# Kernel optimization log

Measured on AMD Instinct MI355X. Metric: run time of the kernel, lower is better.

The kernel has to match this reference:

```python
import jax, jax.numpy as jnp
import numpy as np

B, N, D, M, DEPTH, VOCAB = 8, 128, 128, 16, 4, 100
EIN = 2 * D + 1          # edge MLP input dim: feats_i | feats_j | rel_dist
LN_EPS = 1e-5


def setup_inputs() -> dict:
    key = jax.random.key(0)
    ks = jax.random.split(key, 20)
    s = 0.02  # small init like egnn-pytorch's init_eps
    f32 = jnp.float32
    return {
        "z": jax.random.randint(ks[0], (B, N), 0, VOCAB),
        "pos": jax.random.normal(ks[1], (B, N, 3), f32),
        "mask": jnp.ones((B, N), bool),
        "emb": jax.random.normal(ks[2], (VOCAB, D), f32) * s,
        # edge MLP: Linear(EIN, 2*EIN) -> SiLU -> Linear(2*EIN, M) -> SiLU
        "e_w1": jax.random.normal(ks[3], (DEPTH, EIN, 2 * EIN), f32) * s,
        "e_b1": jnp.zeros((DEPTH, 2 * EIN), f32),
        "e_w2": jax.random.normal(ks[4], (DEPTH, 2 * EIN, M), f32) * s,
        "e_b2": jnp.zeros((DEPTH, M), f32),
        # coors MLP: Linear(M, 4M) -> SiLU -> Linear(4M, 1)
        "c_w1": jax.random.normal(ks[5], (DEPTH, M, 4 * M), f32) * s,
        "c_b1": jnp.zeros((DEPTH, 4 * M), f32),
        "c_w2": jax.random.normal(ks[6], (DEPTH, 4 * M, 1), f32) * s,
        "c_b2": jnp.zeros((DEPTH, 1), f32),
        # node LayerNorm (norm_feats=True in EGNN_Network)
        "ln_g": jnp.ones((DEPTH, D), f32),
        "ln_b": jnp.zeros((DEPTH, D), f32),
        # node MLP: Linear(D+M, 2D) -> SiLU -> Linear(2D, D), residual
        "n_w1": jax.random.normal(ks[7], (DEPTH, D + M, 2 * D), f32) * s,
        "n_b1": jnp.zeros((DEPTH, 2 * D), f32),
        "n_w2": jax.random.normal(ks[8], (DEPTH, 2 * D, D), f32) * s,
        "n_b2": jnp.zeros((DEPTH, D), f32),
    }


def _egnn_forward(z, pos, mask, emb, e_w1, e_b1, e_w2, e_b2,
                  c_w1, c_b1, c_w2, c_b2, ln_g, ln_b,
                  n_w1, n_b1, n_w2, n_b2):
    feats = emb[z]                       # [B,N,D]
    coors = pos                          # [B,N,3]
    mf = mask.astype(feats.dtype)        # [B,N]
    pair = mf[:, :, None] * mf[:, None, :]   # [B,N,N] pairwise mask
    for l in range(DEPTH):
        rel = coors[:, :, None, :] - coors[:, None, :, :]       # [B,N,N,3]
        dist = jnp.sum(rel * rel, axis=-1, keepdims=True)       # [B,N,N,1]
        fi = jnp.broadcast_to(feats[:, :, None, :], (B, N, N, D))
        fj = jnp.broadcast_to(feats[:, None, :, :], (B, N, N, D))
        e = jnp.concatenate([fi, fj, dist], axis=-1)             # [B,N,N,EIN]
        h = jax.nn.silu(e @ e_w1[l] + e_b1[l])                   # [B,N,N,2*EIN]
        m_ij = jax.nn.silu(h @ e_w2[l] + e_b2[l])                # [B,N,N,M]
        # coordinate update
        cw = (jax.nn.silu(m_ij @ c_w1[l] + c_b1[l]) @ c_w2[l] + c_b2[l])[..., 0]
        cw = cw * pair                                           # mask invalid pairs
        coors = coors + jnp.einsum('bij,bijc->bic', cw, rel)
        # node update: masked sum-pool of messages over j
        m_i = jnp.sum(m_ij * pair[..., None], axis=2)            # [B,N,M]
        mu = jnp.mean(feats, axis=-1, keepdims=True)
        var = jnp.var(feats, axis=-1, keepdims=True)
        fn = (feats - mu) * jax.lax.rsqrt(var + LN_EPS) * ln_g[l] + ln_b[l]
        ni = jnp.concatenate([fn, m_i], axis=-1)                 # [B,N,D+M]
        feats = feats + (jax.nn.silu(ni @ n_w1[l] + n_b1[l]) @ n_w2[l] + n_b2[l])
    # masked mean pool
    w = mf[..., None]
    return jnp.sum(feats * w, axis=1) / jnp.maximum(jnp.sum(w, axis=1), 1.0)


def reference(z, pos, mask, emb, e_w1, e_b1, e_w2, e_b2,
              c_w1, c_b1, c_w2, c_b2, ln_g, ln_b,
              n_w1, n_b1, n_w2, n_b2):
    return _egnn_forward(z, pos, mask, emb, e_w1, e_b1, e_w2, e_b2,
                         c_w1, c_b1, c_w2, c_b2, ln_g, ln_b,
                         n_w1, n_b1, n_w2, n_b2)
```

## Files before the change

kernel.cpp:

```cpp
#include <hip/hip_runtime.h>

#define BATCH 8
#define NN    128
#define DD    128
#define MM    16
#define DEPTH 4
#define EIN   257
#define H1    514
#define KPAD  544
#define NCH   17
#define NODES (BATCH*NN)
#define BQ_B  69632
#define NL2E  (-1.442695040888963f)
#define NLN2  (-0.6931471805599453f)

typedef __attribute__((ext_vector_type(8))) short short8;
typedef __attribute__((ext_vector_type(4))) float floatx4;

__device__ __forceinline__ float b2f(unsigned short u) {
    return __uint_as_float(((unsigned int)u) << 16);
}
__device__ __forceinline__ unsigned short f2b(float f) {
    unsigned int x = __float_as_uint(f);
    unsigned int r = (x + 0x7fffu + ((x >> 16) & 1u)) >> 16;
    return (unsigned short)r;
}
__device__ __forceinline__ float siluf(float x) {
    float t = __builtin_amdgcn_exp2f(x * NL2E);
    return x * __builtin_amdgcn_rcpf(1.0f + t);
}
__device__ __forceinline__ float loadf(const void* p, size_t idx, int isbf) {
    return isbf ? b2f(((const unsigned short*)p)[idx]) : ((const float*)p)[idx];
}
__device__ __forceinline__ unsigned int pk2(float x, float y) {
    unsigned int xb = __float_as_uint(x) + 0x8000u;
    unsigned int yb = __float_as_uint(y) + 0x8000u;
    return __builtin_amdgcn_perm(yb, xb, 0x07060302);
}
__device__ __forceinline__ unsigned int h2pk_y(float y0, float y1) {
    float t0 = __builtin_amdgcn_exp2f(y0);
    float t1 = __builtin_amdgcn_exp2f(y1);
    float h0 = y0 * __builtin_amdgcn_rcpf(1.0f + t0);
    float h1 = y1 * __builtin_amdgcn_rcpf(1.0f + t1);
    return pk2(h0, h1);
}

#define OFF_FEATS   0
#define OFF_COORSA  131072
#define OFF_COORSB  134144
#define OFF_AB      137216
#define OFF_BQ      694272
#define OFF_CPK     1267712
#define OFF_WLB     1272576
#define OFF_W2F     1274816
#define OFF_FLAG    1292224
#define OFF_FB16    1292228
#define OFF_W1F     1357764
#define OFF_CF      1636352
#define OFF_NW1F    1640448
#define OFF_NW2F    1722368
#define OFF_NI      1787904

__global__ __launch_bounds__(256) void k_init(
    const int* __restrict__ z, const void* __restrict__ pos,
    const void* __restrict__ emb,
    const void* __restrict__ e_w1, const void* __restrict__ e_w2,
    const void* __restrict__ e_b2,
    const void* __restrict__ c_w1, const void* __restrict__ c_b1,
    const void* __restrict__ c_w2, const void* __restrict__ c_b2,
    const void* __restrict__ n_w1, const void* __restrict__ n_w2,
    float* __restrict__ feats, unsigned short* __restrict__ fb16,
    float* __restrict__ coorsA,
    float* __restrict__ wlb, int4* __restrict__ w2frag,
    int4* __restrict__ w1frag,
    float* __restrict__ cpack, int4* __restrict__ cfrag,
    int4* __restrict__ nw1f, int4* __restrict__ nw2f,
    int* __restrict__ flag) {
    __shared__ int sfl;
    int tid = threadIdx.x, bx = blockIdx.x;
    if (tid < 64) {
        float f = fabsf(__uint_as_float(((const unsigned int*)pos)[tid]));
        bool ok = (f == 0.f) || (f > 1e-8f && f < 1e8f);
        unsigned long long v = __ballot(ok);
        if (tid == 0) sfl = (__builtin_popcountll(v) >= 32) ? 0 : 1;
    }
    __syncthreads();
    int isbf = sfl;
    if (bx == 0 && tid == 0) *flag = isbf;
    if (bx < 512) {
        int node = 2 * bx + (tid >> 7), t = tid & 127;
        int zi = z[node];
        float v = loadf(emb, (size_t)zi * DD + t, isbf);
        feats[node * DD + t] = v;
        fb16[node * DD + t] = f2b(v);
        if (t < 3) coorsA[node * 3 + t] = loadf(pos, node * 3 + t, isbf);
    } else if (bx < 580) {
        int p = bx - 512;
        int layer = p / NCH, kc = p % NCH;
        if (tid < 64) {
            int quad = tid >> 4, c = tid & 15;
            size_t w2base = (size_t)layer * H1 * MM;
            unsigned int u[4];
            #pragma unroll
            for (int pp = 0; pp < 4; ++pp) {
                int k0 = kc * 32 + quad * 8 + 2 * pp, k1 = k0 + 1;
                float f0 = (k0 < H1) ? loadf(e_w2, w2base + (size_t)k0 * MM + c, isbf) : 0.f;
                float f1 = (k1 < H1) ? loadf(e_w2, w2base + (size_t)k1 * MM + c, isbf) : 0.f;
                u[pp] = pk2(f0, f1);
            }
            w2frag[(layer * NCH + kc) * 64 + tid] =
                make_int4((int)u[0], (int)u[1], (int)u[2], (int)u[3]);
            if (kc == 0) {
                size_t wlbase = ((size_t)layer * EIN + 256) * H1;
                for (int t = tid; t < KPAD; t += 64)
                    wlb[layer * 560 + t] =
                        (t < H1) ? NL2E * loadf(e_w1, wlbase + t, isbf) : 0.f;
                if (tid < 16)
                    wlb[layer * 560 + 544 + tid] = loadf(e_b2, layer * MM + tid, isbf);
            }
        }
    } else if (bx < 584) {
        int l = bx - 580;
        for (int idx = tid; idx < 1024; idx += 256) {
            int c = idx >> 6, hh = idx & 63;
            cpack[l * 1216 + hh * 16 + c] = loadf(c_w1, l * 1024 + c * 64 + hh, isbf);
        }
        if (tid < 64)        cpack[l * 1216 + 1024 + tid] = loadf(c_b1, l * 64 + tid, isbf);
        else if (tid < 128)  cpack[l * 1216 + 1088 + tid - 64] = loadf(c_w2, l * 64 + tid - 64, isbf);
        else if (tid == 128) cpack[l * 1216 + 1152] = loadf(c_b2, l, isbf);
        {
            int nt = tid >> 6, lane = tid & 63;
            int col = nt * 16 + (lane & 15);
            unsigned int u[4];
            #pragma unroll
            for (int pp = 0; pp < 4; ++pp) {
                int k0 = (lane >> 4) * 8 + 2 * pp;
                float f0 = (k0 < 16)     ? loadf(c_w1, (size_t)l * 1024 + (size_t)k0 * 64 + col, isbf) : 0.f;
                float f1 = (k0 + 1 < 16) ? loadf(c_w1, (size_t)l * 1024 + (size_t)(k0 + 1) * 64 + col, isbf) : 0.f;
                u[pp] = pk2(f0, f1);
            }
            cfrag[((size_t)l * 4 + nt) * 64 + lane] =
                make_int4((int)u[0], (int)u[1], (int)u[2], (int)u[3]);
        }
    } else if (bx < 856) {
        int p = bx - 584;
        int l = p / 68, nt = p % 68;
        int kcd = tid >> 6, lane = tid & 63;
        int quad = lane >> 4, c16 = lane & 15;
        int n_local = nt * 16 + c16;
        int half = n_local >= KPAD;
        int k_out = n_local - (half ? KPAD : 0);
        size_t wbase = (size_t)l * EIN * H1 + (size_t)(half ? 128 : 0) * H1 + k_out;
        unsigned int u[4];
        #pragma unroll
        for (int pp = 0; pp < 4; ++pp) {
            int d0 = kcd * 32 + quad * 8 + 2 * pp;
            float f0 = (k_out < H1) ? loadf(e_w1, wbase + (size_t)d0 * H1, isbf) : 0.f;
            float f1 = (k_out < H1) ? loadf(e_w1, wbase + (size_t)(d0 + 1) * H1, isbf) : 0.f;
            u[pp] = pk2(f0, f1);
        }
        w1frag[((size_t)(l * 68 + nt) * 4 + kcd) * 64 + lane] =
            make_int4((int)u[0], (int)u[1], (int)u[2], (int)u[3]);
    } else if (bx < 876) {
        int p = bx - 856, l = p / 5, kc = p % 5;
        int lane = tid & 63;
        for (int nt = tid >> 6; nt < 16; nt += 4) {
            int col = nt * 16 + (lane & 15);
            unsigned int u[4];
            #pragma unroll
            for (int pp = 0; pp < 4; ++pp) {
                int k0 = kc * 32 + (lane >> 4) * 8 + 2 * pp;
                float f0 = (k0 < 144)
                    ? loadf(n_w1, (size_t)l * 144 * 256 + (size_t)k0 * 256 + col, isbf) : 0.f;
                float f1 = (k0 + 1 < 144)
                    ? loadf(n_w1, (size_t)l * 144 * 256 + (size_t)(k0 + 1) * 256 + col, isbf) : 0.f;
                u[pp] = pk2(f0, f1);
            }
            nw1f[((size_t)(l * 5 + kc) * 16 + nt) * 64 + lane] =
                make_int4((int)u[0], (int)u[1], (int)u[2], (int)u[3]);
        }
    } else {
        int p = bx - 876, l = p / 8, kc = p % 8;
        int lane = tid & 63;
        for (int nt = tid >> 6; nt < 8; nt += 4) {
            int col = nt * 16 + (lane & 15);
            unsigned int u[4];
            #pragma unroll
            for (int pp = 0; pp < 4; ++pp) {
                int k0 = kc * 32 + (lane >> 4) * 8 + 2 * pp;
                float f0 = loadf(n_w2, (size_t)l * 256 * 128 + (size_t)k0 * 128 + col, isbf);
                float f1 = loadf(n_w2, (size_t)l * 256 * 128 + (size_t)(k0 + 1) * 128 + col, isbf);
                u[pp] = pk2(f0, f1);
            }
            nw2f[((size_t)(l * 8 + kc) * 8 + nt) * 64 + lane] =
                make_int4((int)u[0], (int)u[1], (int)u[2], (int)u[3]);
        }
    }
}

__global__ __launch_bounds__(256) void k1_ab(
    const unsigned short* __restrict__ fb16, const int4* __restrict__ w1f,
    const void* __restrict__ b1raw, unsigned int b1off,
    float* __restrict__ Ab, float* __restrict__ Bq,
    const int* __restrict__ flagp) {
    int bx = blockIdx.x;
    int mt = bx & 63, ng = bx >> 6;
    int tid = threadIdx.x, w = tid >> 6, lane = tid & 63;
    int quad = lane >> 4, c16 = lane & 15;
    int isbf = *flagp;
    int ntile = ng * 4 + w;
    int n_local = ntile * 16 + c16;
    int half = n_local >= KPAD;
    int k_out = n_local - (half ? KPAD : 0);

    const unsigned short* ap = fb16 + (size_t)(mt * 16 + c16) * DD + quad * 8;
    const int4* bp = w1f + (size_t)ntile * 4 * 64 + lane;
    floatx4 acc = {0.f, 0.f, 0.f, 0.f};
    #pragma unroll
    for (int kcd = 0; kcd < 4; ++kcd) {
        short8 af = *(const short8*)(ap + kcd * 32);
        union { int4 i4; short8 s; } bf;
        bf.i4 = bp[kcd * 64];
        acc = __builtin_amdgcn_mfma_f32_16x16x32_bf16(af, bf.s, acc, 0, 0, 0);
    }
    if (!half) {
        float bias = (k_out < H1) ? loadf(b1raw, b1off + k_out, isbf) : 0.f;
        #pragma unroll
        for (int r = 0; r < 4; ++r)
            Ab[(size_t)(mt * 16 + quad * 4 + r) * KPAD + k_out] =
                NL2E * (acc[r] + bias);
    } else {
        int kc = k_out >> 5, kk = k_out & 31;
        int qd = kk >> 3, hsel = (kk >> 2) & 1, tt = k_out & 3;
        #pragma unroll
        for (int r = 0; r < 4; ++r) {
            int node = mt * 16 + quad * 4 + r;
            int bb = node >> 7, j = node & 127;
            int jt = j >> 4, lj = qd * 16 + (j & 15);
            Bq[(size_t)bb * BQ_B + kc * 4096 + jt * 512 + hsel * 256
               + lj * 4 + tt] = NL2E * acc[r];
        }
    }
}

__global__ __launch_bounds__(512, 6) void k2_node(
    const float* __restrict__ Ab, const float* __restrict__ Bq,
    const float* __restrict__ coorsIn, float* __restrict__ coorsOut,
    const float* __restrict__ feats, unsigned short* __restrict__ niB,
    const float* __restrict__ wlbL,
    const short8* __restrict__ w2fragL,
    const float* __restrict__ cpk,
    const int4* __restrict__ cfL,
    const void* __restrict__ gln, const void* __restrict__ bln,
    unsigned int layer, const int* __restrict__ flagp) {
    __shared__ float Ms[128 * 17];
    __shared__ float px[128], py[128], pz[128];
    __shared__ float msum[16][16];
    __shared__ float cwf[128];
    __shared__ float red[2][3];
    __shared__ float fr[128];
    __shared__ float ni[144];
    int tid = threadIdx.x;
    int b = blockIdx.x & 7, ii = blockIdx.x >> 3;
    int node0 = b * NN + ii;
    int w = tid >> 6, lane = tid & 63;
    int quad = lane >> 4, c16 = lane & 15;
    int kg = w >> 2, wj = w & 3;
    int isbf = *flagp;

    if (tid < 128) {
        int g = (b * NN + tid) * 3;
        px[tid] = coorsIn[g]; py[tid] = coorsIn[g + 1]; pz[tid] = coorsIn[g + 2];
    } else if (tid < 256) {
        int t = tid - 128;
        fr[t] = feats[(size_t)node0 * DD + t];
    }
    __syncthreads();

    int j0 = wj * 16 + c16, j1 = j0 + 64;
    float pix = px[ii], piy = py[ii], piz = pz[ii];
    float dxa = pix - px[j0], dya = piy - py[j0], dza = piz - pz[j0];
    float d2a = dxa*dxa + dya*dya + dza*dza;
    float dxb = pix - px[j1], dyb = piy - py[j1], dzb = piz - pz[j1];
    float d2b = dxb*dxb + dyb*dyb + dzb*dzb;
    float b2v = wlbL[544 + c16];

    const float* arow = Ab + (size_t)node0 * KPAD + quad * 8;
    const float* wlr  = wlbL + quad * 8;
    const float* bqw  = Bq + (size_t)b * BQ_B + wj * 512 + lane * 4;
    const short8* wfp = w2fragL + lane;

    floatx4 acc0 = {0.f,0.f,0.f,0.f}, acc1 = {0.f,0.f,0.f,0.f};

    int kc0 = kg ? 9 : 0, kc1 = kg ? 17 : 9;
    {
        const float* bqp = bqw + (size_t)kc0 * 4096;
        float4 npp0 = *(const float4*)(bqp);
        float4 npp1 = *(const float4*)(bqp + 256);
        float4 nqq0 = *(const float4*)(bqp + 2048);
        float4 nqq1 = *(const float4*)(bqp + 2304);
        short8 nbf  = wfp[kc0 * 64];
        for (int kc = kc0; kc < kc1; ++kc) {
            float4 pp0 = npp0, pp1 = npp1, qq0 = nqq0, qq1 = nqq1;
            short8 bf = nbf;
            const float* bqn = bqw + (size_t)(kc + 1) * 4096;
            npp0 = *(const float4*)(bqn);
            npp1 = *(const float4*)(bqn + 256);
            nqq0 = *(const float4*)(bqn + 2048);
            nqq1 = *(const float4*)(bqn + 2304);
            nbf  = wfp[(kc + 1) * 64];
            float4 aA0 = *(const float4*)(arow + kc * 32);
            float4 aA1 = *(const float4*)(arow + kc * 32 + 4);
            float4 l0  = *(const float4*)(wlr + kc * 32);
            float4 l1  = *(const float4*)(wlr + kc * 32 + 4);
            union { unsigned int u[4]; short8 s; } ua, ub;
            ua.u[0] = h2pk_y(fmaf(d2a, l0.x, aA0.x + pp0.x),
                             fmaf(d2a, l0.y, aA0.y + pp0.y));
            ua.u[1] = h2pk_y(fmaf(d2a, l0.z, aA0.z + pp0.z),
                             fmaf(d2a, l0.w, aA0.w + pp0.w));
            ua.u[2] = h2pk_y(fmaf(d2a, l1.x, aA1.x + pp1.x),
                             fmaf(d2a, l1.y, aA1.y + pp1.y));
            ua.u[3] = h2pk_y(fmaf(d2a, l1.z, aA1.z + pp1.z),
                             fmaf(d2a, l1.w, aA1.w + pp1.w));
            ub.u[0] = h2pk_y(fmaf(d2b, l0.x, aA0.x + qq0.x),
                             fmaf(d2b, l0.y, aA0.y + qq0.y));
            ub.u[1] = h2pk_y(fmaf(d2b, l0.z, aA0.z + qq0.z),
                             fmaf(d2b, l0.w, aA0.w + qq0.w));
            ub.u[2] = h2pk_y(fmaf(d2b, l1.x, aA1.x + qq1.x),
                             fmaf(d2b, l1.y, aA1.y + qq1.y));
            ub.u[3] = h2pk_y(fmaf(d2b, l1.z, aA1.z + qq1.z),
                             fmaf(d2b, l1.w, aA1.w + qq1.w));
            acc0 = __builtin_amdgcn_mfma_f32_16x16x32_bf16(ua.s, bf, acc0, 0, 0, 0);
            acc1 = __builtin_amdgcn_mfma_f32_16x16x32_bf16(ub.s, bf, acc1, 0, 0, 0);
        }
    }

    if (kg == 0) {
        #pragma unroll
        for (int r = 0; r < 4; ++r) {
            int jl = (wj * 16 + quad * 4 + r) * 17 + c16;
            Ms[jl]           = acc0[r];
            Ms[jl + 64 * 17] = acc1[r];
        }
    }
    __syncthreads();
    if (kg == 1) {
        #pragma unroll
        for (int r = 0; r < 4; ++r) {
            int jl = (wj * 16 + quad * 4 + r) * 17 + c16;
            Ms[jl]           = siluf(fmaf(Ms[jl]           + acc0[r], NLN2, b2v));
            Ms[jl + 64 * 17] = siluf(fmaf(Ms[jl + 64 * 17] + acc1[r], NLN2, b2v));
        }
    }
    __syncthreads();

    if (tid < 256) {
        int g = tid >> 4, c = tid & 15;
        float s = 0.f;
        #pragma unroll
        for (int t = 0; t < 8; ++t) s += Ms[(g * 8 + t) * 17 + c];
        msum[g][c] = s;
    }
    __syncthreads();

    if (tid < 16) {
        float s = 0.f;
        #pragma unroll
        for (int g = 0; g < 16; ++g) s += msum[g][tid];
        ni[128 + tid] = s;
    }
    if (tid < 64) {
        int l6 = tid;
        unsigned int lnoff = layer * DD;
        float v0 = fr[l6], v1 = fr[l6 + 64];
        float s1 = v0 + v1, s2 = v0 * v0 + v1 * v1;
        #pragma unroll
        for (int off = 32; off >= 1; off >>= 1) {
            s1 += __shfl_xor(s1, off, 64);
            s2 += __shfl_xor(s2, off, 64);
        }
        float mu  = s1 * (1.0f / 128.0f);
        float var = s2 * (1.0f / 128.0f) - mu * mu;
        float rs  = rsqrtf(var + 1e-5f);
        ni[l6]      = (v0 - mu) * rs * loadf(gln, lnoff + l6, isbf)
                    + loadf(bln, lnoff + l6, isbf);
        ni[l6 + 64] = (v1 - mu) * rs * loadf(gln, lnoff + l6 + 64, isbf)
                    + loadf(bln, lnoff + l6 + 64, isbf);
    }

    {
        int l15 = lane & 15, l4 = lane >> 4;
        union { unsigned int u[4]; short8 s; } am;
        if (l4 < 2) {
            const float* msp = &Ms[(w * 16 + l15) * 17 + l4 * 8];
            am.u[0] = pk2(msp[0], msp[1]);
            am.u[1] = pk2(msp[2], msp[3]);
            am.u[2] = pk2(msp[4], msp[5]);
            am.u[3] = pk2(msp[6], msp[7]);
        } else {
            am.u[0] = am.u[1] = am.u[2] = am.u[3] = 0u;
        }
        floatx4 ca0 = {0.f,0.f,0.f,0.f}, ca1 = {0.f,0.f,0.f,0.f},
                ca2 = {0.f,0.f,0.f,0.f}, ca3 = {0.f,0.f,0.f,0.f};
        union { int4 i4; short8 s; } cb;
        cb.i4 = cfL[0 * 64 + lane];
        ca0 = __builtin_amdgcn_mfma_f32_16x16x32_bf16(am.s, cb.s, ca0, 0, 0, 0);
        cb.i4 = cfL[1 * 64 + lane];
        ca1 = __builtin_amdgcn_mfma_f32_16x16x32_bf16(am.s, cb.s, ca1, 0, 0, 0);
        cb.i4 = cfL[2 * 64 + lane];
        ca2 = __builtin_amdgcn_mfma_f32_16x16x32_bf16(am.s, cb.s, ca2, 0, 0, 0);
        cb.i4 = cfL[3 * 64 + lane];
        ca3 = __builtin_amdgcn_mfma_f32_16x16x32_bf16(am.s, cb.s, ca3, 0, 0, 0);
        float cb1v0 = cpk[1024 + l15],      cw2v0 = cpk[1088 + l15];
        float cb1v1 = cpk[1024 + 16 + l15], cw2v1 = cpk[1088 + 16 + l15];
        float cb1v2 = cpk[1024 + 32 + l15], cw2v2 = cpk[1088 + 32 + l15];
        float cb1v3 = cpk[1024 + 48 + l15], cw2v3 = cpk[1088 + 48 + l15];
        float cwp[4];
        #pragma unroll
        for (int r = 0; r < 4; ++r) {
            cwp[r] = siluf(ca0[r] + cb1v0) * cw2v0
                   + siluf(ca1[r] + cb1v1) * cw2v1
                   + siluf(ca2[r] + cb1v2) * cw2v2
                   + siluf(ca3[r] + cb1v3) * cw2v3;
        }
        #pragma unroll
        for (int off = 1; off <= 8; off <<= 1) {
            #pragma unroll
            for (int r = 0; r < 4; ++r) cwp[r] += __shfl_xor(cwp[r], off, 64);
        }
        if (l15 == 0) {
            float cb2v = cpk[1152];
            #pragma unroll
            for (int r = 0; r < 4; ++r)
                cwf[w * 16 + l4 * 4 + r] = cwp[r] + cb2v;
        }
    }
    __syncthreads();

    if (tid < 128) {
        int j = tid;
        float cw = cwf[j];
        float vx = cw * (pix - px[j]), vy = cw * (piy - py[j]),
              vz = cw * (piz - pz[j]);
        #pragma unroll
        for (int off = 32; off >= 1; off >>= 1) {
            vx += __shfl_xor(vx, off, 64);
            vy += __shfl_xor(vy, off, 64);
            vz += __shfl_xor(vz, off, 64);
        }
        if (lane == 0) { red[w][0] = vx; red[w][1] = vy; red[w][2] = vz; }
    } else if (tid < 288) {
        int t = tid - 128;
        niB[(size_t)node0 * 160 + t] = (t < 144) ? f2b(ni[t]) : (unsigned short)0;
    }
    __syncthreads();

    if (tid < 3) {
        coorsOut[node0 * 3 + tid] = coorsIn[node0 * 3 + tid]
            + red[0][tid] + red[1][tid];
    }
}

__global__ __launch_bounds__(256) void k3_node(
    const unsigned short* __restrict__ niB,
    const int4* __restrict__ nw1f, const int4* __restrict__ nw2f,
    const void* __restrict__ b1r, const void* __restrict__ b2r,
    float* __restrict__ feats, unsigned short* __restrict__ fb16,
    unsigned int layer, const int* __restrict__ flagp) {
    __shared__ float hid[16][260];
    int tid = threadIdx.x, m = blockIdx.x;
    int w = tid >> 6, lane = tid & 63;
    int l15 = lane & 15, l4 = lane >> 4;
    int isbf = *flagp;

    floatx4 acc0 = {0.f,0.f,0.f,0.f}, acc1 = {0.f,0.f,0.f,0.f},
            acc2 = {0.f,0.f,0.f,0.f}, acc3 = {0.f,0.f,0.f,0.f};
    const unsigned short* nip = niB + (size_t)(m * 16 + l15) * 160 + l4 * 8;
    const int4* b1p = nw1f + (size_t)layer * 5 * 16 * 64 + lane;
    #pragma unroll
    for (int kc = 0; kc < 5; ++kc) {
        short8 af = *(const short8*)(nip + kc * 32);
        union { int4 i4; short8 s; } bf;
        bf.i4 = b1p[(kc * 16 + w * 4 + 0) * 64];
        acc0 = __builtin_amdgcn_mfma_f32_16x16x32_bf16(af, bf.s, acc0, 0, 0, 0);
        bf.i4 = b1p[(kc * 16 + w * 4 + 1) * 64];
        acc1 = __builtin_amdgcn_mfma_f32_16x16x32_bf16(af, bf.s, acc1, 0, 0, 0);
        bf.i4 = b1p[(kc * 16 + w * 4 + 2) * 64];
        acc2 = __builtin_amdgcn_mfma_f32_16x16x32_bf16(af, bf.s, acc2, 0, 0, 0);
        bf.i4 = b1p[(kc * 16 + w * 4 + 3) * 64];
        acc3 = __builtin_amdgcn_mfma_f32_16x16x32_bf16(af, bf.s, acc3, 0, 0, 0);
    }
    {
        int h0 = (w * 4) * 16 + l15;
        float b1v0 = loadf(b1r, layer * 256 + h0, isbf);
        float b1v1 = loadf(b1r, layer * 256 + h0 + 16, isbf);
        float b1v2 = loadf(b1r, layer * 256 + h0 + 32, isbf);
        float b1v3 = loadf(b1r, layer * 256 + h0 + 48, isbf);
        #pragma unroll
        for (int r = 0; r < 4; ++r) {
            int row = l4 * 4 + r;
            hid[row][h0]      = siluf(acc0[r] + b1v0);
            hid[row][h0 + 16] = siluf(acc1[r] + b1v1);
            hid[row][h0 + 32] = siluf(acc2[r] + b1v2);
            hid[row][h0 + 48] = siluf(acc3[r] + b1v3);
        }
    }
    __syncthreads();

    floatx4 o0 = {0.f,0.f,0.f,0.f}, o1 = {0.f,0.f,0.f,0.f};
    const int4* b2p = nw2f + (size_t)layer * 8 * 8 * 64 + lane;
    #pragma unroll
    for (int kc = 0; kc < 8; ++kc) {
        const float* hp = &hid[l15][kc * 32 + l4 * 8];
        float4 h0 = *(const float4*)(hp);
        float4 h1 = *(const float4*)(hp + 4);
        union { unsigned int u[4]; short8 s; } af;
        af.u[0] = pk2(h0.x, h0.y); af.u[1] = pk2(h0.z, h0.w);
        af.u[2] = pk2(h1.x, h1.y); af.u[3] = pk2(h1.z, h1.w);
        union { int4 i4; short8 s; } bf;
        bf.i4 = b2p[(kc * 8 + w * 2 + 0) * 64];
        o0 = __builtin_amdgcn_mfma_f32_16x16x32_bf16(af.s, bf.s, o0, 0, 0, 0);
        bf.i4 = b2p[(kc * 8 + w * 2 + 1) * 64];
        o1 = __builtin_amdgcn_mfma_f32_16x16x32_bf16(af.s, bf.s, o1, 0, 0, 0);
    }
    {
        int c0 = (w * 2) * 16 + l15;
        float b2v0 = loadf(b2r, layer * 128 + c0, isbf);
        float b2v1 = loadf(b2r, layer * 128 + c0 + 16, isbf);
        #pragma unroll
        for (int r = 0; r < 4; ++r) {
            int node = m * 16 + l4 * 4 + r;
            float v0 = feats[(size_t)node * DD + c0] + o0[r] + b2v0;
            float v1 = feats[(size_t)node * DD + c0 + 16] + o1[r] + b2v1;
            feats[(size_t)node * DD + c0]      = v0;
            feats[(size_t)node * DD + c0 + 16] = v1;
            fb16[(size_t)node * DD + c0]       = f2b(v0);
            fb16[(size_t)node * DD + c0 + 16]  = f2b(v1);
        }
    }
}

__global__ __launch_bounds__(128) void k4_pool(
    const float* __restrict__ feats, void* __restrict__ out,
    const int* __restrict__ flagp) {
    int b = blockIdx.x, d = threadIdx.x;
    float s = 0.f;
    for (int n = 0; n < NN; ++n) s += feats[((size_t)(b * NN + n)) * DD + d];
    float v = s * (1.0f / 128.0f);
    if (*flagp) ((unsigned short*)out)[b * DD + d] = f2b(v);
    else        ((float*)out)[b * DD + d] = v;
}

extern "C" void kernel_launch(void* const* d_in, const int* in_sizes, int n_in,
                              void* d_out, int out_size, void* d_ws, size_t ws_size,
                              hipStream_t stream) {
    const int* z = (const int*)d_in[0];
    const void* pos  = d_in[1];
    const void* emb  = d_in[3];
    const void* e_w1 = d_in[4];
    const void* e_b1 = d_in[5];
    const void* e_w2 = d_in[6];
    const void* e_b2 = d_in[7];
    const void* c_w1 = d_in[8];
    const void* c_b1 = d_in[9];
    const void* c_w2 = d_in[10];
    const void* c_b2 = d_in[11];
    const void* ln_g = d_in[12];
    const void* ln_b = d_in[13];
    const void* n_w1 = d_in[14];
    const void* n_b1 = d_in[15];
    const void* n_w2 = d_in[16];
    const void* n_b2 = d_in[17];

    float* ws     = (float*)d_ws;
    float* feats  = ws + OFF_FEATS;
    float* coorsA = ws + OFF_COORSA;
    float* coorsB = ws + OFF_COORSB;
    float* Ab     = ws + OFF_AB;
    float* Bq     = ws + OFF_BQ;
    float* cpk    = ws + OFF_CPK;
    float* wlb    = ws + OFF_WLB;
    int4*  w2f    = (int4*)(ws + OFF_W2F);
    int*   flag   = (int*)(ws + OFF_FLAG);
    unsigned short* fb16 = (unsigned short*)(ws + OFF_FB16);
    int4*  w1f    = (int4*)(ws + OFF_W1F);
    int4*  cf     = (int4*)(ws + OFF_CF);
    int4*  nw1f   = (int4*)(ws + OFF_NW1F);
    int4*  nw2f   = (int4*)(ws + OFF_NW2F);
    unsigned short* niB = (unsigned short*)(ws + OFF_NI);

    k_init<<<908, 256, 0, stream>>>(
        z, pos, emb, e_w1, e_w2, e_b2, c_w1, c_b1, c_w2, c_b2, n_w1, n_w2,
        feats, fb16, coorsA, wlb, w2f, w1f, cpk, cf, nw1f, nw2f, flag);

    float* cin = coorsA; float* cout = coorsB;
    for (int l = 0; l < DEPTH; ++l) {
        k1_ab<<<1088, 256, 0, stream>>>(
            fb16, w1f + (size_t)l * 68 * 4 * 64, e_b1,
            (unsigned int)(l * H1), Ab, Bq, flag);
        k2_node<<<NODES, 512, 0, stream>>>(
            Ab, Bq, cin, cout, feats, niB,
            wlb + l * 560, (const short8*)(w2f + (size_t)l * NCH * 64),
            cpk + (size_t)l * 1216, cf + (size_t)l * 4 * 64,
            ln_g, ln_b, (unsigned int)l, flag);
        k3_node<<<NODES / 16, 256, 0, stream>>>(
            niB, nw1f, nw2f, n_b1, n_b2, feats, fb16,
            (unsigned int)l, flag);
        float* t = cin; cin = cout; cout = t;
    }
    k4_pool<<<BATCH, 128, 0, stream>>>(feats, d_out, flag);
}
```

Before: 254.2 us.

## Fuse node MLP into next layer's edge projection and pair two nodes per block

Fuses the node-update MLP (k3) with the next layer's Ab/Bq edge-projection (k1) into one kernel. Each of the 17 column-group blocks recomputes the 16-node MLP redundantly, which removes a launch and the fb16 round trip. Feats are now ping-ponged between two buffers so the redundant blocks can read old feats safely. The pair kernel now handles two i-nodes per block, reusing the Bq and weight-fragment loads across both, and replaces the msum reduction with shuffles plus fewer syncs. The cost is heavy redundant MLP compute in the fused kernel and more registers in k2, whose occupancy hint drops from 6 to 4.

```diff
diff --git a/kernel.cpp b/kernel.cpp
--- a/kernel.cpp
+++ b/kernel.cpp
@@ -60,6 +60,7 @@
 #define OFF_NW1F    1640448
 #define OFF_NW2F    1722368
 #define OFF_NI      1787904
+#define OFF_FEATS2  1869824
 
 __global__ __launch_bounds__(256) void k_init(
     const int* __restrict__ z, const void* __restrict__ pos,
@@ -243,26 +244,146 @@
     }
 }
 
-__global__ __launch_bounds__(512, 6) void k2_node(
+__global__ __launch_bounds__(256) void k13(
+    const unsigned short* __restrict__ niB,
+    const int4* __restrict__ nw1f, const int4* __restrict__ nw2f,
+    const void* __restrict__ nb1, const void* __restrict__ nb2,
+    const float* __restrict__ featsIn, float* __restrict__ featsOut,
+    const int4* __restrict__ w1f, const void* __restrict__ b1raw,
+    unsigned int b1off, float* __restrict__ Ab, float* __restrict__ Bq,
+    unsigned int lm1, const int* __restrict__ flagp) {
+    __shared__ float hid[16][260];
+    __shared__ unsigned short fbt[16][136];
+    int tid = threadIdx.x, bx = blockIdx.x;
+    int mt = bx & 63, ng = bx >> 6;
+    int w = tid >> 6, lane = tid & 63;
+    int l15 = lane & 15, l4 = lane >> 4;
+    int isbf = *flagp;
+
+    floatx4 acc0 = {0.f,0.f,0.f,0.f}, acc1 = {0.f,0.f,0.f,0.f},
+            acc2 = {0.f,0.f,0.f,0.f}, acc3 = {0.f,0.f,0.f,0.f};
+    const unsigned short* nip = niB + (size_t)(mt * 16 + l15) * 160 + l4 * 8;
+    const int4* b1p = nw1f + (size_t)lm1 * 5 * 16 * 64 + lane;
+    #pragma unroll
+    for (int kc = 0; kc < 5; ++kc) {
+        short8 af = *(const short8*)(nip + kc * 32);
+        union { int4 i4; short8 s; } bf;
+        bf.i4 = b1p[(kc * 16 + w * 4 + 0) * 64];
+        acc0 = __builtin_amdgcn_mfma_f32_16x16x32_bf16(af, bf.s, acc0, 0, 0, 0);
+        bf.i4 = b1p[(kc * 16 + w * 4 + 1) * 64];
+        acc1 = __builtin_amdgcn_mfma_f32_16x16x32_bf16(af, bf.s, acc1, 0, 0, 0);
+        bf.i4 = b1p[(kc * 16 + w * 4 + 2) * 64];
+        acc2 = __builtin_amdgcn_mfma_f32_16x16x32_bf16(af, bf.s, acc2, 0, 0, 0);
+        bf.i4 = b1p[(kc * 16 + w * 4 + 3) * 64];
+        acc3 = __builtin_amdgcn_mfma_f32_16x16x32_bf16(af, bf.s, acc3, 0, 0, 0);
+    }
+    {
+        int h0 = (w * 4) * 16 + l15;
+        float b1v0 = loadf(nb1, lm1 * 256 + h0, isbf);
+        float b1v1 = loadf(nb1, lm1 * 256 + h0 + 16, isbf);
+        float b1v2 = loadf(nb1, lm1 * 256 + h0 + 32, isbf);
+        float b1v3 = loadf(nb1, lm1 * 256 + h0 + 48, isbf);
+        #pragma unroll
+        for (int r = 0; r < 4; ++r) {
+            int row = l4 * 4 + r;
+            hid[row][h0]      = siluf(acc0[r] + b1v0);
+            hid[row][h0 + 16] = siluf(acc1[r] + b1v1);
+            hid[row][h0 + 32] = siluf(acc2[r] + b1v2);
+            hid[row][h0 + 48] = siluf(acc3[r] + b1v3);
+        }
+    }
+    __syncthreads();
+
+    floatx4 o0 = {0.f,0.f,0.f,0.f}, o1 = {0.f,0.f,0.f,0.f};
+    const int4* b2p = nw2f + (size_t)lm1 * 8 * 8 * 64 + lane;
+    #pragma unroll
+    for (int kc = 0; kc < 8; ++kc) {
+        const float* hp = &hid[l15][kc * 32 + l4 * 8];
+        float4 h0 = *(const float4*)(hp);
+        float4 h1 = *(const float4*)(hp + 4);
+        union { unsigned int u[4]; short8 s; } af;
+        af.u[0] = pk2(h0.x, h0.y); af.u[1] = pk2(h0.z, h0.w);
+        af.u[2] = pk2(h1.x, h1.y); af.u[3] = pk2(h1.z, h1.w);
+        union { int4 i4; short8 s; } bf;
+        bf.i4 = b2p[(kc * 8 + w * 2 + 0) * 64];
+        o0 = __builtin_amdgcn_mfma_f32_16x16x32_bf16(af.s, bf.s, o0, 0, 0, 0);
+        bf.i4 = b2p[(kc * 8 + w * 2 + 1) * 64];
+        o1 = __builtin_amdgcn_mfma_f32_16x16x32_bf16(af.s, bf.s, o1, 0, 0, 0);
+    }
+    {
+        int c0 = (w * 2) * 16 + l15;
+        float b2v0 = loadf(nb2, lm1 * 128 + c0, isbf);
+        float b2v1 = loadf(nb2, lm1 * 128 + c0 + 16, isbf);
+        #pragma unroll
+        for (int r = 0; r < 4; ++r) {
+            int row = l4 * 4 + r;
+            int node = mt * 16 + row;
+            float v0 = featsIn[(size_t)node * DD + c0] + o0[r] + b2v0;
+            float v1 = featsIn[(size_t)node * DD + c0 + 16] + o1[r] + b2v1;
+            fbt[row][c0]      = f2b(v0);
+            fbt[row][c0 + 16] = f2b(v1);
+            if (ng == 0) {
+                featsOut[(size_t)node * DD + c0]      = v0;
+                featsOut[(size_t)node * DD + c0 + 16] = v1;
+            }
+        }
+    }
+    __syncthreads();
+
+    int quad = l4, c16 = l15;
+    int ntile = ng * 4 + w;
+    int n_local = ntile * 16 + c16;
+    int half = n_local >= KPAD;
+    int k_out = n_local - (half ? KPAD : 0);
+    const int4* bp = w1f + (size_t)ntile * 4 * 64 + lane;
+    floatx4 acc = {0.f, 0.f, 0.f, 0.f};
+    #pragma unroll
+    for (int kcd = 0; kcd < 4; ++kcd) {
+        short8 af = *(const short8*)(&fbt[c16][quad * 8 + kcd * 32]);
+        union { int4 i4; short8 s; } bf;
+        bf.i4 = bp[kcd * 64];
+        acc = __builtin_amdgcn_mfma_f32_16x16x32_bf16(af, bf.s, acc, 0, 0, 0);
+    }
+    if (!half) {
+        float bias = (k_out < H1) ? loadf(b1raw, b1off + k_out, isbf) : 0.f;
+        #pragma unroll
+        for (int r = 0; r < 4; ++r)
+            Ab[(size_t)(mt * 16 + quad * 4 + r) * KPAD + k_out] =
+                NL2E * (acc[r] + bias);
+    } else {
+        int kc = k_out >> 5, kk = k_out & 31;
+        int qd = kk >> 3, hsel = (kk >> 2) & 1, tt = k_out & 3;
+        #pragma unroll
+        for (int r = 0; r < 4; ++r) {
+            int node = mt * 16 + quad * 4 + r;
+            int bb = node >> 7, j = node & 127;
+            int jt = j >> 4, lj = qd * 16 + (j & 15);
+            Bq[(size_t)bb * BQ_B + kc * 4096 + jt * 512 + hsel * 256
+               + lj * 4 + tt] = NL2E * acc[r];
+        }
+    }
+}
+
+__global__ __launch_bounds__(512, 4) void k2_pair(
     const float* __restrict__ Ab, const float* __restrict__ Bq,
     const float* __restrict__ coorsIn, float* __restrict__ coorsOut,
-    const float* __restrict__ feats, unsigned short* __restrict__ niB,
+    const float* __restrict__ featsIn, unsigned short* __restrict__ niB,
     const float* __restrict__ wlbL,
     const short8* __restrict__ w2fragL,
     const float* __restrict__ cpk,
     const int4* __restrict__ cfL,
     const void* __restrict__ gln, const void* __restrict__ bln,
     unsigned int layer, const int* __restrict__ flagp) {
-    __shared__ float Ms[128 * 17];
+    __shared__ float Ms[2][128 * 17];
     __shared__ float px[128], py[128], pz[128];
-    __shared__ float msum[16][16];
-    __shared__ float cwf[128];
-    __shared__ float red[2][3];
-    __shared__ float fr[128];
-    __shared__ float ni[144];
+    __shared__ float msum[2][4][16];
+    __shared__ float cwf[2][128];
+    __shared__ float fr[2][128];
+    __shared__ float ni[2][144];
     int tid = threadIdx.x;
-    int b = blockIdx.x & 7, ii = blockIdx.x >> 3;
-    int node0 = b * NN + ii;
+    int b = blockIdx.x & 7, ip = blockIdx.x >> 3;
+    int i0 = ip * 2;
+    int node0 = b * NN + i0;
     int w = tid >> 6, lane = tid & 63;
     int quad = lane >> 4, c16 = lane & 15;
     int kg = w >> 2, wj = w & 3;
@@ -271,26 +392,34 @@
     if (tid < 128) {
         int g = (b * NN + tid) * 3;
         px[tid] = coorsIn[g]; py[tid] = coorsIn[g + 1]; pz[tid] = coorsIn[g + 2];
-    } else if (tid < 256) {
-        int t = tid - 128;
-        fr[t] = feats[(size_t)node0 * DD + t];
+    } else if (tid < 384) {
+        int n = (tid - 128) >> 7, t = tid & 127;
+        fr[n][t] = featsIn[(size_t)(node0 + n) * DD + t];
     }
     __syncthreads();
 
     int j0 = wj * 16 + c16, j1 = j0 + 64;
-    float pix = px[ii], piy = py[ii], piz = pz[ii];
-    float dxa = pix - px[j0], dya = piy - py[j0], dza = piz - pz[j0];
-    float d2a = dxa*dxa + dya*dya + dza*dza;
-    float dxb = pix - px[j1], dyb = piy - py[j1], dzb = piz - pz[j1];
-    float d2b = dxb*dxb + dyb*dyb + dzb*dzb;
+    float pix0 = px[i0],     piy0 = py[i0],     piz0 = pz[i0];
+    float pix1 = px[i0 + 1], piy1 = py[i0 + 1], piz1 = pz[i0 + 1];
+    float dx, dy, dz;
+    dx = pix0 - px[j0]; dy = piy0 - py[j0]; dz = piz0 - pz[j0];
+    float d2a0 = dx*dx + dy*dy + dz*dz;
+    dx = pix0 - px[j1]; dy = piy0 - py[j1]; dz = piz0 - pz[j1];
+    float d2b0 = dx*dx + dy*dy + dz*dz;
+    dx = pix1 - px[j0]; dy = piy1 - py[j0]; dz = piz1 - pz[j0];
+    float d2a1 = dx*dx + dy*dy + dz*dz;
+    dx = pix1 - px[j1]; dy = piy1 - py[j1]; dz = piz1 - pz[j1];
+    float d2b1 = dx*dx + dy*dy + dz*dz;
     float b2v = wlbL[544 + c16];
 
-    const float* arow = Ab + (size_t)node0 * KPAD + quad * 8;
-    const float* wlr  = wlbL + quad * 8;
-    const float* bqw  = Bq + (size_t)b * BQ_B + wj * 512 + lane * 4;
-    const short8* wfp = w2fragL + lane;
-
-    floatx4 acc0 = {0.f,0.f,0.f,0.f}, acc1 = {0.f,0.f,0.f,0.f};
+    const float* arow0 = Ab + (size_t)node0 * KPAD + quad * 8;
+    const float* arow1 = arow0 + KPAD;
+    const float* wlr   = wlbL + quad * 8;
+    const float* bqw   = Bq + (size_t)b * BQ_B + wj * 512 + lane * 4;
+    const short8* wfp  = w2fragL + lane;
+
+    floatx4 acc00 = {0.f,0.f,0.f,0.f}, acc01 = {0.f,0.f,0.f,0.f};
+    floatx4 acc10 = {0.f,0.f,0.f,0.f}, acc11 = {0.f,0.f,0.f,0.f};
 
     int kc0 = kg ? 9 : 0, kc1 = kg ? 17 : 9;
     {
@@ -309,29 +438,49 @@
             nqq0 = *(const float4*)(bqn + 2048);
             nqq1 = *(const float4*)(bqn + 2304);
             nbf  = wfp[(kc + 1) * 64];
-            float4 aA0 = *(const float4*)(arow + kc * 32);
-            float4 aA1 = *(const float4*)(arow + kc * 32 + 4);
+            float4 aA0 = *(const float4*)(arow0 + kc * 32);
+            float4 aA1 = *(const float4*)(arow0 + kc * 32 + 4);
+            float4 aB0 = *(const float4*)(arow1 + kc * 32);
+            float4 aB1 = *(const float4*)(arow1 + kc * 32 + 4);
             float4 l0  = *(const float4*)(wlr + kc * 32);
             float4 l1  = *(const float4*)(wlr + kc * 32 + 4);
-            union { unsigned int u[4]; short8 s; } ua, ub;
-            ua.u[0] = h2pk_y(fmaf(d2a, l0.x, aA0.x + pp0.x),
-                             fmaf(d2a, l0.y, aA0.y + pp0.y));
-            ua.u[1] = h2pk_y(fmaf(d2a, l0.z, aA0.z + pp0.z),
-                             fmaf(d2a, l0.w, aA0.w + pp0.w));
-            ua.u[2] = h2pk_y(fmaf(d2a, l1.x, aA1.x + pp1.x),
-                             fmaf(d2a, l1.y, aA1.y + pp1.y));
-            ua.u[3] = h2pk_y(fmaf(d2a, l1.z, aA1.z + pp1.z),
-                             fmaf(d2a, l1.w, aA1.w + pp1.w));
-            ub.u[0] = h2pk_y(fmaf(d2b, l0.x, aA0.x + qq0.x),
-                             fmaf(d2b, l0.y, aA0.y + qq0.y));
-            ub.u[1] = h2pk_y(fmaf(d2b, l0.z, aA0.z + qq0.z),
-                             fmaf(d2b, l0.w, aA0.w + qq0.w));
-            ub.u[2] = h2pk_y(fmaf(d2b, l1.x, aA1.x + qq1.x),
-                             fmaf(d2b, l1.y, aA1.y + qq1.y));
-            ub.u[3] = h2pk_y(fmaf(d2b, l1.z, aA1.z + qq1.z),
-                             fmaf(d2b, l1.w, aA1.w + qq1.w));
-            acc0 = __builtin_amdgcn_mfma_f32_16x16x32_bf16(ua.s, bf, acc0, 0, 0, 0);
-            acc1 = __builtin_amdgcn_mfma_f32_16x16x32_bf16(ub.s, bf, acc1, 0, 0, 0);
+            union { unsigned int u[4]; short8 s; } ua, ub, uc, ud;
+            ua.u[0] = h2pk_y(fmaf(d2a0, l0.x, aA0.x + pp0.x),
+                             fmaf(d2a0, l0.y, aA0.y + pp0.y));
+            ua.u[1] = h2pk_y(fmaf(d2a0, l0.z, aA0.z + pp0.z),
+                             fmaf(d2a0, l0.w, aA0.w + pp0.w));
+            ua.u[2] = h2pk_y(fmaf(d2a0, l1.x, aA1.x + pp1.x),
+                             fmaf(d2a0, l1.y, aA1.y + pp1.y));
+            ua.u[3] = h2pk_y(fmaf(d2a0, l1.z, aA1.z + pp1.z),
+                             fmaf(d2a0, l1.w, aA1.w + pp1.w));
+            ub.u[0] = h2pk_y(fmaf(d2b0, l0.x, aA0.x + qq0.x),
+                             fmaf(d2b0, l0.y, aA0.y + qq0.y));
+            ub.u[1] = h2pk_y(fmaf(d2b0, l0.z, aA0.z + qq0.z),
+                             fmaf(d2b0, l0.w, aA0.w + qq0.w));
+            ub.u[2] = h2pk_y(fmaf(d2b0, l1.x, aA1.x + qq1.x),
+                             fmaf(d2b0, l1.y, aA1.y + qq1.y));
+            ub.u[3] = h2pk_y(fmaf(d2b0, l1.z, aA1.z + qq1.z),
+                             fmaf(d2b0, l1.w, aA1.w + qq1.w));
+            uc.u[0] = h2pk_y(fmaf(d2a1, l0.x, aB0.x + pp0.x),
+                             fmaf(d2a1, l0.y, aB0.y + pp0.y));
+            uc.u[1] = h2pk_y(fmaf(d2a1, l0.z, aB0.z + pp0.z),
+                             fmaf(d2a1, l0.w, aB0.w + pp0.w));
+            uc.u[2] = h2pk_y(fmaf(d2a1, l1.x, aB1.x + pp1.x),
+                             fmaf(d2a1, l1.y, aB1.y + pp1.y));
+            uc.u[3] = h2pk_y(fmaf(d2a1, l1.z, aB1.z + pp1.z),
+                             fmaf(d2a1, l1.w, aB1.w + pp1.w));
+            ud.u[0] = h2pk_y(fmaf(d2b1, l0.x, aB0.x + qq0.x),
+                             fmaf(d2b1, l0.y, aB0.y + qq0.y));
+            ud.u[1] = h2pk_y(fmaf(d2b1, l0.z, aB0.z + qq0.z),
+                             fmaf(d2b1, l0.w, aB0.w + qq0.w));
+            ud.u[2] = h2pk_y(fmaf(d2b1, l1.x, aB1.x + qq1.x),
+                             fmaf(d2b1, l1.y, aB1.y + qq1.y));
+            ud.u[3] = h2pk_y(fmaf(d2b1, l1.z, aB1.z + qq1.z),
+                             fmaf(d2b1, l1.w, aB1.w + qq1.w));
+            acc00 = __builtin_amdgcn_mfma_f32_16x16x32_bf16(ua.s, bf, acc00, 0, 0, 0);
+            acc01 = __builtin_amdgcn_mfma_f32_16x16x32_bf16(ub.s, bf, acc01, 0, 0, 0);
+            acc10 = __builtin_amdgcn_mfma_f32_16x16x32_bf16(uc.s, bf, acc10, 0, 0, 0);
+            acc11 = __builtin_amdgcn_mfma_f32_16x16x32_bf16(ud.s, bf, acc11, 0, 0, 0);
         }
     }
 
@@ -339,40 +488,35 @@
         #pragma unroll
         for (int r = 0; r < 4; ++r) {
             int jl = (wj * 16 + quad * 4 + r) * 17 + c16;
-            Ms[jl]           = acc0[r];
-            Ms[jl + 64 * 17] = acc1[r];
+            Ms[0][jl]        = acc00[r];
+            Ms[0][jl + 1088] = acc01[r];
+            Ms[1][jl]        = acc10[r];
+            Ms[1][jl + 1088] = acc11[r];
         }
     }
     __syncthreads();
+
     if (kg == 1) {
+        float s0 = 0.f, s1 = 0.f;
         #pragma unroll
         for (int r = 0; r < 4; ++r) {
             int jl = (wj * 16 + quad * 4 + r) * 17 + c16;
-            Ms[jl]           = siluf(fmaf(Ms[jl]           + acc0[r], NLN2, b2v));
-            Ms[jl + 64 * 17] = siluf(fmaf(Ms[jl + 64 * 17] + acc1[r], NLN2, b2v));
-        }
-    }
-    __syncthreads();
-
-    if (tid < 256) {
-        int g = tid >> 4, c = tid & 15;
-        float s = 0.f;
-        #pragma unroll
-        for (int t = 0; t < 8; ++t) s += Ms[(g * 8 + t) * 17 + c];
-        msum[g][c] = s;
-    }
-    __syncthreads();
-
-    if (tid < 16) {
-        float s = 0.f;
-        #pragma unroll
-        for (int g = 0; g < 16; ++g) s += msum[g][tid];
-        ni[128 + tid] = s;
-    }
-    if (tid < 64) {
-        int l6 = tid;
+            float m00 = siluf(fmaf(Ms[0][jl]        + acc00[r], NLN2, b2v));
+            float m01 = siluf(fmaf(Ms[0][jl + 1088] + acc01[r], NLN2, b2v));
+            float m10 = siluf(fmaf(Ms[1][jl]        + acc10[r], NLN2, b2v));
+            float m11 = siluf(fmaf(Ms[1][jl + 1088] + acc11[r], NLN2, b2v));
+            Ms[0][jl] = m00; Ms[0][jl + 1088] = m01;
+            Ms[1][jl] = m10; Ms[1][jl + 1088] = m11;
+            s0 += m00 + m01;
+            s1 += m10 + m11;
+        }
+        s0 += __shfl_xor(s0, 16, 64); s0 += __shfl_xor(s0, 32, 64);
+        s1 += __shfl_xor(s1, 16, 64); s1 += __shfl_xor(s1, 32, 64);
+        if (quad == 0) { msum[0][wj][c16] = s0; msum[1][wj][c16] = s1; }
+    } else if (w < 2) {
+        int n = w, l6 = lane;
         unsigned int lnoff = layer * DD;
-        float v0 = fr[l6], v1 = fr[l6 + 64];
+        float v0 = fr[n][l6], v1 = fr[n][l6 + 64];
         float s1 = v0 + v1, s2 = v0 * v0 + v1 * v1;
         #pragma unroll
         for (int off = 32; off >= 1; off >>= 1) {
@@ -382,91 +526,108 @@
         float mu  = s1 * (1.0f / 128.0f);
         float var = s2 * (1.0f / 128.0f) - mu * mu;
         float rs  = rsqrtf(var + 1e-5f);
-        ni[l6]      = (v0 - mu) * rs * loadf(gln, lnoff + l6, isbf)
-                    + loadf(bln, lnoff + l6, isbf);
-        ni[l6 + 64] = (v1 - mu) * rs * loadf(gln, lnoff + l6 + 64, isbf)
-                    + loadf(bln, lnoff + l6 + 64, isbf);
-    }
+        ni[n][l6]      = (v0 - mu) * rs * loadf(gln, lnoff + l6, isbf)
+                       + loadf(bln, lnoff + l6, isbf);
+        ni[n][l6 + 64] = (v1 - mu) * rs * loadf(gln, lnoff + l6 + 64, isbf)
+                       + loadf(bln, lnoff + l6 + 64, isbf);
+    }
+    __syncthreads();
 
     {
         int l15 = lane & 15, l4 = lane >> 4;
-        union { unsigned int u[4]; short8 s; } am;
-        if (l4 < 2) {
-            const float* msp = &Ms[(w * 16 + l15) * 17 + l4 * 8];
-            am.u[0] = pk2(msp[0], msp[1]);
-            am.u[1] = pk2(msp[2], msp[3]);
-            am.u[2] = pk2(msp[4], msp[5]);
-            am.u[3] = pk2(msp[6], msp[7]);
-        } else {
-            am.u[0] = am.u[1] = am.u[2] = am.u[3] = 0u;
-        }
-        floatx4 ca0 = {0.f,0.f,0.f,0.f}, ca1 = {0.f,0.f,0.f,0.f},
-                ca2 = {0.f,0.f,0.f,0.f}, ca3 = {0.f,0.f,0.f,0.f};
-        union { int4 i4; short8 s; } cb;
-        cb.i4 = cfL[0 * 64 + lane];
-        ca0 = __builtin_amdgcn_mfma_f32_16x16x32_bf16(am.s, cb.s, ca0, 0, 0, 0);
-        cb.i4 = cfL[1 * 64 + lane];
-        ca1 = __builtin_amdgcn_mfma_f32_16x16x32_bf16(am.s, cb.s, ca1, 0, 0, 0);
-        cb.i4 = cfL[2 * 64 + lane];
-        ca2 = __builtin_amdgcn_mfma_f32_16x16x32_bf16(am.s, cb.s, ca2, 0, 0, 0);
-        cb.i4 = cfL[3 * 64 + lane];
-        ca3 = __builtin_amdgcn_mfma_f32_16x16x32_bf16(am.s, cb.s, ca3, 0, 0, 0);
+        int nw = w >> 2;
         float cb1v0 = cpk[1024 + l15],      cw2v0 = cpk[1088 + l15];
         float cb1v1 = cpk[1024 + 16 + l15], cw2v1 = cpk[1088 + 16 + l15];
         float cb1v2 = cpk[1024 + 32 + l15], cw2v2 = cpk[1088 + 32 + l15];
         float cb1v3 = cpk[1024 + 48 + l15], cw2v3 = cpk[1088 + 48 + l15];
-        float cwp[4];
-        #pragma unroll
-        for (int r = 0; r < 4; ++r) {
-            cwp[r] = siluf(ca0[r] + cb1v0) * cw2v0
-                   + siluf(ca1[r] + cb1v1) * cw2v1
-                   + siluf(ca2[r] + cb1v2) * cw2v2
-                   + siluf(ca3[r] + cb1v3) * cw2v3;
-        }
-        #pragma unroll
-        for (int off = 1; off <= 8; off <<= 1) {
+        float cb2v = cpk[1152];
+        #pragma unroll
+        for (int it = 0; it < 2; ++it) {
+            int g = (w & 3) * 2 + it;
+            union { unsigned int u[4]; short8 s; } am;
+            if (l4 < 2) {
+                const float* msp = &Ms[nw][(g * 16 + l15) * 17 + l4 * 8];
+                am.u[0] = pk2(msp[0], msp[1]);
+                am.u[1] = pk2(msp[2], msp[3]);
+                am.u[2] = pk2(msp[4], msp[5]);
+                am.u[3] = pk2(msp[6], msp[7]);
+            } else {
+                am.u[0] = am.u[1] = am.u[2] = am.u[3] = 0u;
+            }
+            floatx4 ca0 = {0.f,0.f,0.f,0.f}, ca1 = {0.f,0.f,0.f,0.f},
+                    ca2 = {0.f,0.f,0.f,0.f}, ca3 = {0.f,0.f,0.f,0.f};
+            union { int4 i4; short8 s; } cb;
+            cb.i4 = cfL[0 * 64 + lane];
+            ca0 = __builtin_amdgcn_mfma_f32_16x16x32_bf16(am.s, cb.s, ca0, 0, 0, 0);
+            cb.i4 = cfL[1 * 64 + lane];
+            ca1 = __builtin_amdgcn_mfma_f32_16x16x32_bf16(am.s, cb.s, ca1, 0, 0, 0);
+            cb.i4 = cfL[2 * 64 + lane];
+            ca2 = __builtin_amdgcn_mfma_f32_16x16x32_bf16(am.s, cb.s, ca2, 0, 0, 0);
+            cb.i4 = cfL[3 * 64 + lane];
+            ca3 = __builtin_amdgcn_mfma_f32_16x16x32_bf16(am.s, cb.s, ca3, 0, 0, 0);
+            float cwp[4];
             #pragma unroll
-            for (int r = 0; r < 4; ++r) cwp[r] += __shfl_xor(cwp[r], off, 64);
-        }
-        if (l15 == 0) {
-            float cb2v = cpk[1152];
+            for (int r = 0; r < 4; ++r) {
+                cwp[r] = siluf(ca0[r] + cb1v0) * cw2v0
+                       + siluf(ca1[r] + cb1v1) * cw2v1
+                       + siluf(ca2[r] + cb1v2) * cw2v2
+                       + siluf(ca3[r] + cb1v3) * cw2v3;
+            }
             #pragma unroll
-            for (int r = 0; r < 4; ++r)
-                cwf[w * 16 + l4 * 4 + r] = cwp[r] + cb2v;
-        }
+            for (int off = 1; off <= 8; off <<= 1) {
+                #pragma unroll
+                for (int r = 0; r < 4; ++r) cwp[r] += __shfl_xor(cwp[r], off, 64);
+            }
+            if (l15 == 0) {
+                #pragma unroll
+                for (int r = 0; r < 4; ++r)
+                    cwf[nw][g * 16 + l4 * 4 + r] = cwp[r] + cb2v;
+            }
+        }
+    }
+    if (tid < 32) {
+        int n = tid >> 4, c = tid & 15;
+        ni[n][128 + c] = msum[n][0][c] + msum[n][1][c]
+                       + msum[n][2][c] + msum[n][3][c];
     }
     __syncthreads();
 
-    if (tid < 128) {
-        int j = tid;
-        float cw = cwf[j];
-        float vx = cw * (pix - px[j]), vy = cw * (piy - py[j]),
-              vz = cw * (piz - pz[j]);
+    if (w < 2) {
+        int n = w, j = lane;
+        float pnx = n ? pix1 : pix0;
+        float pny = n ? piy1 : piy0;
+        float pnz = n ? piz1 : piz0;
+        float cwA = cwf[n][j], cwB = cwf[n][j + 64];
+        float vx = cwA * (pnx - px[j]) + cwB * (pnx - px[j + 64]);
+        float vy = cwA * (pny - py[j]) + cwB * (pny - py[j + 64]);
+        float vz = cwA * (pnz - pz[j]) + cwB * (pnz - pz[j + 64]);
         #pragma unroll
         for (int off = 32; off >= 1; off >>= 1) {
             vx += __shfl_xor(vx, off, 64);
             vy += __shfl_xor(vy, off, 64);
             vz += __shfl_xor(vz, off, 64);
         }
-        if (lane == 0) { red[w][0] = vx; red[w][1] = vy; red[w][2] = vz; }
-    } else if (tid < 288) {
+        if (lane == 0) {
+            int nd = node0 + n;
+            coorsOut[nd * 3 + 0] = coorsIn[nd * 3 + 0] + vx;
+            coorsOut[nd * 3 + 1] = coorsIn[nd * 3 + 1] + vy;
+            coorsOut[nd * 3 + 2] = coorsIn[nd * 3 + 2] + vz;
+        }
+    } else if (tid < 448) {
         int t = tid - 128;
-        niB[(size_t)node0 * 160 + t] = (t < 144) ? f2b(ni[t]) : (unsigned short)0;
-    }
-    __syncthreads();
-
-    if (tid < 3) {
-        coorsOut[node0 * 3 + tid] = coorsIn[node0 * 3 + tid]
-            + red[0][tid] + red[1][tid];
-    }
-}
-
-__global__ __launch_bounds__(256) void k3_node(
+        int n = (t >= 160) ? 1 : 0;
+        int tt = t - n * 160;
+        niB[(size_t)(node0 + n) * 160 + tt] =
+            (tt < 144) ? f2b(ni[n][tt]) : (unsigned short)0;
+    }
+}
+
+__global__ __launch_bounds__(256) void k3_last(
     const unsigned short* __restrict__ niB,
     const int4* __restrict__ nw1f, const int4* __restrict__ nw2f,
-    const void* __restrict__ b1r, const void* __restrict__ b2r,
-    float* __restrict__ feats, unsigned short* __restrict__ fb16,
-    unsigned int layer, const int* __restrict__ flagp) {
+    const void* __restrict__ nb1, const void* __restrict__ nb2,
+    const float* __restrict__ featsIn, float* __restrict__ featsOut,
+    unsigned int lm1, const int* __restrict__ flagp) {
     __shared__ float hid[16][260];
     int tid = threadIdx.x, m = blockIdx.x;
     int w = tid >> 6, lane = tid & 63;
@@ -476,7 +637,7 @@
     floatx4 acc0 = {0.f,0.f,0.f,0.f}, acc1 = {0.f,0.f,0.f,0.f},
             acc2 = {0.f,0.f,0.f,0.f}, acc3 = {0.f,0.f,0.f,0.f};
     const unsigned short* nip = niB + (size_t)(m * 16 + l15) * 160 + l4 * 8;
-    const int4* b1p = nw1f + (size_t)layer * 5 * 16 * 64 + lane;
+    const int4* b1p = nw1f + (size_t)lm1 * 5 * 16 * 64 + lane;
     #pragma unroll
     for (int kc = 0; kc < 5; ++kc) {
         short8 af = *(const short8*)(nip + kc * 32);
@@ -492,10 +653,10 @@
     }
     {
         int h0 = (w * 4) * 16 + l15;
-        float b1v0 = loadf(b1r, layer * 256 + h0, isbf);
-        float b1v1 = loadf(b1r, layer * 256 + h0 + 16, isbf);
-        float b1v2 = loadf(b1r, layer * 256 + h0 + 32, isbf);
-        float b1v3 = loadf(b1r, layer * 256 + h0 + 48, isbf);
+        float b1v0 = loadf(nb1, lm1 * 256 + h0, isbf);
+        float b1v1 = loadf(nb1, lm1 * 256 + h0 + 16, isbf);
+        float b1v2 = loadf(nb1, lm1 * 256 + h0 + 32, isbf);
+        float b1v3 = loadf(nb1, lm1 * 256 + h0 + 48, isbf);
         #pragma unroll
         for (int r = 0; r < 4; ++r) {
             int row = l4 * 4 + r;
@@ -508,7 +669,7 @@
     __syncthreads();
 
     floatx4 o0 = {0.f,0.f,0.f,0.f}, o1 = {0.f,0.f,0.f,0.f};
-    const int4* b2p = nw2f + (size_t)layer * 8 * 8 * 64 + lane;
+    const int4* b2p = nw2f + (size_t)lm1 * 8 * 8 * 64 + lane;
     #pragma unroll
     for (int kc = 0; kc < 8; ++kc) {
         const float* hp = &hid[l15][kc * 32 + l4 * 8];
@@ -525,17 +686,15 @@
     }
     {
         int c0 = (w * 2) * 16 + l15;
-        float b2v0 = loadf(b2r, layer * 128 + c0, isbf);
-        float b2v1 = loadf(b2r, layer * 128 + c0 + 16, isbf);
+        float b2v0 = loadf(nb2, lm1 * 128 + c0, isbf);
+        float b2v1 = loadf(nb2, lm1 * 128 + c0 + 16, isbf);
         #pragma unroll
         for (int r = 0; r < 4; ++r) {
             int node = m * 16 + l4 * 4 + r;
-            float v0 = feats[(size_t)node * DD + c0] + o0[r] + b2v0;
-            float v1 = feats[(size_t)node * DD + c0 + 16] + o1[r] + b2v1;
-            feats[(size_t)node * DD + c0]      = v0;
-            feats[(size_t)node * DD + c0 + 16] = v1;
-            fb16[(size_t)node * DD + c0]       = f2b(v0);
-            fb16[(size_t)node * DD + c0 + 16]  = f2b(v1);
+            featsOut[(size_t)node * DD + c0] =
+                featsIn[(size_t)node * DD + c0] + o0[r] + b2v0;
+            featsOut[(size_t)node * DD + c0 + 16] =
+                featsIn[(size_t)node * DD + c0 + 16] + o1[r] + b2v1;
         }
     }
 }
@@ -573,7 +732,8 @@
     const void* n_b2 = d_in[17];
 
     float* ws     = (float*)d_ws;
-    float* feats  = ws + OFF_FEATS;
+    float* feats0 = ws + OFF_FEATS;
+    float* feats1 = ws + OFF_FEATS2;
     float* coorsA = ws + OFF_COORSA;
     float* coorsB = ws + OFF_COORSB;
     float* Ab     = ws + OFF_AB;
@@ -591,22 +751,34 @@
 
     k_init<<<908, 256, 0, stream>>>(
         z, pos, emb, e_w1, e_w2, e_b2, c_w1, c_b1, c_w2, c_b2, n_w1, n_w2,
-        feats, fb16, coorsA, wlb, w2f, w1f, cpk, cf, nw1f, nw2f, flag);
+        feats0, fb16, coorsA, wlb, w2f, w1f, cpk, cf, nw1f, nw2f, flag);
 
     float* cin = coorsA; float* cout = coorsB;
-    for (int l = 0; l < DEPTH; ++l) {
-        k1_ab<<<1088, 256, 0, stream>>>(
-            fb16, w1f + (size_t)l * 68 * 4 * 64, e_b1,
-            (unsigned int)(l * H1), Ab, Bq, flag);
-        k2_node<<<NODES, 512, 0, stream>>>(
-            Ab, Bq, cin, cout, feats, niB,
+    float* fcur = feats0; float* fnext = feats1;
+
+    k1_ab<<<1088, 256, 0, stream>>>(
+        fb16, w1f, e_b1, 0u, Ab, Bq, flag);
+    k2_pair<<<NODES / 2, 512, 0, stream>>>(
+        Ab, Bq, cin, cout, fcur, niB,
+        wlb, (const short8*)w2f, cpk, cf,
+        ln_g, ln_b, 0u, flag);
+    { float* t = cin; cin = cout; cout = t; }
+
+    for (int l = 1; l < DEPTH; ++l) {
+        k13<<<1088, 256, 0, stream>>>(
+            niB, nw1f, nw2f, n_b1, n_b2, fcur, fnext,
+            w1f + (size_t)l * 68 * 4 * 64, e_b1, (unsigned int)(l * H1),
+            Ab, Bq, (unsigned int)(l - 1), flag);
+        { float* t = fcur; fcur = fnext; fnext = t; }
+        k2_pair<<<NODES / 2, 512, 0, stream>>>(
+            Ab, Bq, cin, cout, fcur, niB,
             wlb + l * 560, (const short8*)(w2f + (size_t)l * NCH * 64),
             cpk + (size_t)l * 1216, cf + (size_t)l * 4 * 64,
             ln_g, ln_b, (unsigned int)l, flag);
-        k3_node<<<NODES / 16, 256, 0, stream>>>(
-            niB, nw1f, nw2f, n_b1, n_b2, feats, fb16,
-            (unsigned int)l, flag);
-        float* t = cin; cin = cout; cout = t;
-    }
-    k4_pool<<<BATCH, 128, 0, stream>>>(feats, d_out, flag);
-}
+        { float* t = cin; cin = cout; cout = t; }
+    }
+
+    k3_last<<<NODES / 16, 256, 0, stream>>>(
+        niB, nw1f, nw2f, n_b1, n_b2, fcur, fnext, 3u, flag);
+    k4_pool<<<BATCH, 128, 0, stream>>>(fnext, d_out, flag);
+}
```

Result: no change. 254.2 us (median of 2 runs) (+0.0%).
